# Kernel tuning notes

Measured on AMD Instinct MI355X. Metric: run time of the kernel, lower is better.

The kernel has to match this reference:

```python
import jax, jax.numpy as jnp
import numpy as np

D_MODEL = 512
D_INNER = 1024           # expand=2 * d_model
HEADDIM = 1024           # headdim = 2*hidden_dim -> nheads = 1
NHEADS = 1
D_STATE = 128            # Mamba2 default
D_CONV = 4               # Mamba2 default
CONV_DIM = D_INNER + 2 * D_STATE   # 1280
D_IN_PROJ = 2 * D_INNER + 2 * D_STATE + NHEADS  # 2305
BATCH, SEQ = 8, 2048
EPS = 1e-5


def setup_inputs() -> dict:
    key = jax.random.key(0)
    ks = jax.random.split(key, 8)
    x = jax.random.normal(ks[0], (BATCH, SEQ, D_MODEL), dtype=jnp.float32)
    rnn_state = jnp.zeros((1, BATCH, D_MODEL), dtype=jnp.float32)
    W_in = jax.random.normal(ks[1], (D_MODEL, D_IN_PROJ), dtype=jnp.float32) * 0.02
    conv_w = jax.random.normal(ks[2], (CONV_DIM, D_CONV), dtype=jnp.float32) * 0.2
    conv_b = jnp.zeros((CONV_DIM,), dtype=jnp.float32)
    dt_bias = jax.random.normal(ks[3], (NHEADS,), dtype=jnp.float32) * 0.1
    # A in (-16, -1): A_log = log(uniform(1,16))
    A_log = jnp.log(jax.random.uniform(ks[4], (NHEADS,), minval=1.0, maxval=16.0, dtype=jnp.float32))
    D = jnp.ones((NHEADS,), dtype=jnp.float32)
    norm_w = jnp.ones((D_INNER,), dtype=jnp.float32)
    W_out = jax.random.normal(ks[5], (D_INNER, D_MODEL), dtype=jnp.float32) * 0.02
    return {"x": x, "rnn_state": rnn_state, "W_in": W_in, "conv_w": conv_w,
            "conv_b": conv_b, "dt_bias": dt_bias, "A_log": A_log, "D": D,
            "norm_w": norm_w, "W_out": W_out}


def _mamba2_forward(x, W_in, conv_w, conv_b, dt_bias, A_log, D, norm_w, W_out):
    Bsz, T, _ = x.shape
    zxbcdt = x @ W_in                              # [B,T,2305]
    z = zxbcdt[..., :D_INNER]                      # [B,T,1024]
    xBC = zxbcdt[..., D_INNER:D_INNER + CONV_DIM]  # [B,T,1280]
    dt = zxbcdt[..., -NHEADS:]                     # [B,T,1]

    # causal depthwise conv1d over time, then silu
    xBC_t = jnp.transpose(xBC, (0, 2, 1))          # [B,C,T]
    w = conv_w[:, None, :]                          # [C,1,K]
    conv = jax.lax.conv_general_dilated(
        xBC_t, w, window_strides=(1,), padding=[(D_CONV - 1, 0)],
        feature_group_count=CONV_DIM, dimension_numbers=("NCH", "OIH", "NCH"))
    xBC = jax.nn.silu(jnp.transpose(conv, (0, 2, 1)) + conv_b)  # [B,T,1280]

    x_ssm = xBC[..., :D_INNER].reshape(Bsz, T, NHEADS, HEADDIM)  # [B,T,H,P]
    Bm = xBC[..., D_INNER:D_INNER + D_STATE]       # [B,T,N] (ngroups=1)
    Cm = xBC[..., -D_STATE:]                       # [B,T,N]

    dt = jax.nn.softplus(dt + dt_bias)             # [B,T,H]
    A = -jnp.exp(A_log)                            # [H]

    # selective SSM recurrence over time (time-major scan)
    xs = (jnp.transpose(x_ssm, (1, 0, 2, 3)),      # [T,B,H,P]
          jnp.transpose(dt, (1, 0, 2)),            # [T,B,H]
          jnp.transpose(Bm, (1, 0, 2)),            # [T,B,N]
          jnp.transpose(Cm, (1, 0, 2)))            # [T,B,N]
    h0 = jnp.zeros((Bsz, NHEADS, HEADDIM, D_STATE), dtype=x.dtype)

    def step(h, inp):
        xt, dtt, Bt, Ct = inp
        dA = jnp.exp(dtt * A)                      # [B,H]
        h = h * dA[:, :, None, None] + (dtt[:, :, None] * xt)[..., None] * Bt[:, None, None, :]
        y = jnp.einsum("bhpn,bn->bhp", h, Ct)
        return h, y

    _, ys = jax.lax.scan(step, h0, xs)             # ys: [T,B,H,P]
    y = jnp.transpose(ys, (1, 0, 2, 3)) + x_ssm * D[None, None, :, None]
    y = y.reshape(Bsz, T, D_INNER)

    # gated RMSNorm (norm_before_gate=False): rmsnorm(y * silu(z)) * weight
    y = y * jax.nn.silu(z)
    y = y * jax.lax.rsqrt(jnp.mean(y * y, axis=-1, keepdims=True) + EPS) * norm_w
    return y @ W_out                               # [B,T,D_MODEL]


def reference(x, rnn_state, W_in, conv_w, conv_b, dt_bias, A_log, D, norm_w, W_out):
    out = _mamba2_forward(x, W_in, conv_w, conv_b, dt_bias, A_log, D, norm_w, W_out)
    return (out, rnn_state)
```

## Files before the change

kernel.cpp:

```cpp
#include <hip/hip_runtime.h>
#include <hip/hip_bf16.h>
#include <math.h>

#define D_MODEL 512
#define D_INNER 1024
#define D_STATE 128
#define CONV_DIM (D_INNER + 2*D_STATE)
#define D_IN_PROJ (2*D_INNER + 2*D_STATE + 1)
#define NPROJ 2304
#define BATCH 8
#define SEQ 2048
#define NROWS (BATCH*SEQ)
#define CHUNK 128
#define NCHUNK (NROWS/CHUNK)
#define CPB (SEQ/CHUNK)
#define EPS_RMS 1e-5f

typedef __hip_bfloat16 bf16;
typedef __attribute__((ext_vector_type(8))) short short8;
typedef __attribute__((ext_vector_type(4))) float f32x4;

__device__ __forceinline__ float fbf(bf16 v) { return __bfloat162float(v); }
__device__ __forceinline__ bf16 tbf(float v) { return __float2bfloat16(v); }
__device__ __forceinline__ float fexp(float x) { return __expf(x); }
__device__ __forceinline__ float frcp(float x) { return __builtin_amdgcn_rcpf(x); }
__device__ __forceinline__ float fsilu(float a) { return a * frcp(1.f + fexp(-a)); }

__device__ __forceinline__ void gl2lds16(const bf16* g, bf16* l) {
    __builtin_amdgcn_global_load_lds(
        (const __attribute__((address_space(1))) unsigned int*)g,
        (__attribute__((address_space(3))) unsigned int*)l, 16, 0, 0);
}

__global__ __launch_bounds__(256) void k_prologue(
    const float* __restrict__ W_in, const float* __restrict__ W_out,
    const float* __restrict__ norm_w, const float* __restrict__ rnn,
    bf16* __restrict__ W_inbT, bf16* __restrict__ W_outbT, float* __restrict__ outTail)
{
    int b = blockIdx.x;
    if (b == 1152 + 512) {
        int tid = threadIdx.x;
        #pragma unroll
        for (int i = 0; i < 4; ++i)
            *(float4*)(outTail + (tid + i * 256) * 4) =
                *(const float4*)(rnn + (tid + i * 256) * 4);
        return;
    }
    __shared__ float tile[32][33];
    const float* src; bf16* dst; const float* scale;
    int c0, r0, sstride, C;
    if (b < 1152) {
        src = W_in; dst = W_inbT; scale = nullptr;
        c0 = (b % 16) * 32; r0 = (b / 16) * 32; sstride = D_IN_PROJ; C = D_MODEL;
    } else {
        int bb = b - 1152;
        src = W_out; dst = W_outbT; scale = norm_w;
        c0 = (bb % 32) * 32; r0 = (bb / 32) * 32; sstride = D_MODEL; C = D_INNER;
    }
    int tx = threadIdx.x & 31, ty = threadIdx.x >> 5;
    #pragma unroll
    for (int i = 0; i < 32; i += 8) {
        float s = scale ? scale[c0 + ty + i] : 1.f;
        tile[ty + i][tx] = src[(size_t)(c0 + ty + i) * sstride + (r0 + tx)] * s;
    }
    __syncthreads();
    #pragma unroll
    for (int i = 0; i < 32; i += 8)
        dst[(size_t)(r0 + ty + i) * C + (c0 + tx)] = tbf(tile[tx][ty + i]);
}

__global__ __launch_bounds__(256) void k_dtcvt(
    const float* __restrict__ x, const float* __restrict__ W_in,
    const float* __restrict__ dt_bias,
    bf16* __restrict__ xb, float* __restrict__ dts, float* __restrict__ ssq)
{
    __shared__ float wcol[D_MODEL];
    int tid = threadIdx.x;
    wcol[tid]       = W_in[(size_t)tid * D_IN_PROJ + 2304];
    wcol[tid + 256] = W_in[(size_t)(tid + 256) * D_IN_PROJ + 2304];
    __syncthreads();
    int row  = blockIdx.x * 4 + (tid >> 6);
    int lane = tid & 63;
    const float* xr = x + (size_t)row * D_MODEL;
    float4 a = *(const float4*)(xr + lane * 8);
    float4 b = *(const float4*)(xr + lane * 8 + 4);
    union { bf16 o[8]; uint4 u; } pk;
    pk.o[0]=tbf(a.x); pk.o[1]=tbf(a.y); pk.o[2]=tbf(a.z); pk.o[3]=tbf(a.w);
    pk.o[4]=tbf(b.x); pk.o[5]=tbf(b.y); pk.o[6]=tbf(b.z); pk.o[7]=tbf(b.w);
    *(uint4*)(xb + (size_t)row * D_MODEL + lane * 8) = pk.u;
    const float* wc = wcol + lane * 8;
    float s = a.x*wc[0]+a.y*wc[1]+a.z*wc[2]+a.w*wc[3]
            + b.x*wc[4]+b.y*wc[5]+b.z*wc[6]+b.w*wc[7];
    #pragma unroll
    for (int off = 32; off; off >>= 1) s += __shfl_xor(s, off);
    if (lane == 0) {
        float raw = s + dt_bias[0];
        dts[row] = raw > 20.f ? raw : log1pf(fexp(raw));
        ssq[row] = 0.f;
    }
}

template<int MODE>
__global__ __launch_bounds__(256) void k_bgemm(
    const bf16* __restrict__ A, int lda, size_t sA,
    const bf16* __restrict__ Bt, int ldb, size_t sB,
    void* __restrict__ Cv, int ldc, size_t sC, int K,
    const bf16* __restrict__ zg, float* __restrict__ ssq)
{
    constexpr int BK = 64;
    __shared__ __align__(16) bf16 SM[4 * 8192];
    const int tid = threadIdx.x, lane = tid & 63, wave = tid >> 6;
    const int wm = (wave & 1) * 64, wn = (wave >> 1) * 64;
    const int lr = lane & 15, quad = lane >> 4;
    const int rx = lr & 7;
    size_t bm, bn;
    if (MODE == 3) { bm = (size_t)blockIdx.y * 128; bn = (size_t)blockIdx.x * 128; }
    else           { bm = (size_t)blockIdx.x * 128; bn = (size_t)blockIdx.y * 128; }
    const size_t bi = blockIdx.z;
    A  += bi * sA;
    Bt += bi * sB;
    const int srow = lane >> 3;
    const int scol = (((lane & 7) ^ srow) << 3);

    f32x4 acc[4][4];
    #pragma unroll
    for (int i = 0; i < 4; ++i)
        #pragma unroll
        for (int j = 0; j < 4; ++j) acc[i][j] = (f32x4){0.f,0.f,0.f,0.f};

    auto stage = [&](bf16* Ad, bf16* Bd, int k0) {
        #pragma unroll
        for (int q = 0; q < 4; ++q) {
            int rg = wave * 32 + q * 8;
            gl2lds16(A  + (bm + rg + srow) * lda + k0 + scol, Ad + rg * BK);
            gl2lds16(Bt + (bn + rg + srow) * ldb + k0 + scol, Bd + rg * BK);
        }
    };

    const int NT = K / BK;
    stage(SM, SM + 8192, 0);
    if (NT > 1) stage(SM + 16384, SM + 24576, BK);

    for (int kt = 0; kt < NT; ++kt) {
        if (kt + 1 < NT) asm volatile("s_waitcnt vmcnt(8)" ::: "memory");
        else             asm volatile("s_waitcnt vmcnt(0)" ::: "memory");
        __builtin_amdgcn_s_barrier();
        __builtin_amdgcn_sched_barrier(0);
        const bf16* As = SM + (kt & 1) * 16384;
        const bf16* Bs = As + 8192;
        #pragma unroll
        for (int ks = 0; ks < BK; ks += 32) {
            const int off = ((((ks >> 3) + quad) ^ rx) << 3);
            short8 af[4], bg[4];
            #pragma unroll
            for (int i = 0; i < 4; ++i)
                af[i] = *(const short8*)(As + (wm + i*16 + lr) * BK + off);
            #pragma unroll
            for (int j = 0; j < 4; ++j)
                bg[j] = *(const short8*)(Bs + (wn + j*16 + lr) * BK + off);
            #pragma unroll
            for (int i = 0; i < 4; ++i)
                #pragma unroll
                for (int j = 0; j < 4; ++j)
                    acc[i][j] = __builtin_amdgcn_mfma_f32_16x16x32_bf16(af[i], bg[j], acc[i][j], 0,0,0);
        }
        __builtin_amdgcn_sched_barrier(0);
        __builtin_amdgcn_s_barrier();
        if (kt + 2 < NT) {
            bf16* An = SM + (kt & 1) * 16384;
            stage(An, An + 8192, (kt + 2) * BK);
        }
    }
    if (MODE <= 1) {
        #pragma unroll
        for (int i = 0; i < 4; ++i)
            #pragma unroll
            for (int j = 0; j < 4; ++j)
                #pragma unroll
                for (int r = 0; r < 4; ++r) {
                    size_t row = bm + wm + i*16 + quad*4 + r;
                    size_t col = bn + wn + j*16 + lr;
                    float v = acc[i][j][r];
                    if (MODE == 0) ((float*)Cv + bi*sC)[row * ldc + col] = v;
                    else           ((bf16*)Cv + bi*sC)[row * ldc + col] = tbf(v);
                }
    } else if (MODE == 2) {
        const size_t tokbase = bi * CHUNK;
        const bf16* zrow = zg + tokbase * D_INNER + bn;
        __syncthreads();
        #pragma unroll
        for (int q = 0; q < 8; ++q) {
            int r0 = wave * 32 + q * 4;
            int rr = r0 + (lane >> 4);
            int gl = (lane & 15) ^ (rr & 7);
            gl2lds16(zrow + (size_t)rr * D_INNER + gl * 8, SM + r0 * 128);
        }
        __syncthreads();
        float srw[4][4];
        #pragma unroll
        for (int i = 0; i < 4; ++i)
            #pragma unroll
            for (int r = 0; r < 4; ++r) srw[i][r] = 0.f;
        #pragma unroll
        for (int i = 0; i < 4; ++i)
            #pragma unroll
            for (int j = 0; j < 4; ++j)
                #pragma unroll
                for (int r = 0; r < 4; ++r) {
                    int row = wm + i*16 + quad*4 + r;
                    int col = wn + j*16 + lr;
                    int gph = ((col >> 3) ^ (row & 7));
                    float z = fbf(SM[row * 128 + (gph << 3) + (col & 7)]);
                    float g = acc[i][j][r] * z * frcp(1.f + fexp(-z));
                    ((bf16*)Cv + bi*sC)[(size_t)row * ldc + bn + col] = tbf(g);
                    srw[i][r] += g * g;
                }
        #pragma unroll
        for (int i = 0; i < 4; ++i)
            #pragma unroll
            for (int r = 0; r < 4; ++r) {
                float s = srw[i][r];
                s += __shfl_xor(s, 1);
                s += __shfl_xor(s, 2);
                s += __shfl_xor(s, 4);
                s += __shfl_xor(s, 8);
                if (lr == 0)
                    atomicAdd(ssq + tokbase + wm + i*16 + quad*4 + r, s);
            }
    } else {
        #pragma unroll
        for (int i = 0; i < 4; ++i)
            #pragma unroll
            for (int r = 0; r < 4; ++r) {
                size_t row = bm + wm + i*16 + quad*4 + r;
                float sc = rsqrtf(ssq[row] * (1.f / D_INNER) + EPS_RMS);
                #pragma unroll
                for (int j = 0; j < 4; ++j) {
                    size_t col = bn + wn + j*16 + lr;
                    ((float*)Cv + bi*sC)[row * ldc + col] = acc[i][j][r] * sc;
                }
            }
    }
}

__global__ __launch_bounds__(256) void k_gemm_in(
    const bf16* __restrict__ A, const bf16* __restrict__ Bt,
    bf16* __restrict__ zb, bf16* __restrict__ xBCin)
{
    constexpr int BK = 64;
    constexpr int K = D_MODEL;
    constexpr int NT = K / BK;
    __shared__ __align__(16) bf16 SM[4 * 8192];
    const int tid = threadIdx.x, lane = tid & 63, wave = tid >> 6;
    const int wm = (wave & 1) * 64, wn = (wave >> 1) * 64;
    const int lr = lane & 15, quad = lane >> 4;
    const int rx = lr & 7;
    const int bid = blockIdx.x;
    const int xcd = bid & 7, lid = bid >> 3;
    const int st  = lid / 72, r5 = lid % 72;
    const size_t bm = (size_t)(xcd * 16 + st * 4 + r5 / 18) * 128;
    const int    bn = (r5 % 18) * 128;
    const int srow = lane >> 3;
    const int scol = (((lane & 7) ^ srow) << 3);

    f32x4 acc[4][4];
    #pragma unroll
    for (int i = 0; i < 4; ++i)
        #pragma unroll
        for (int j = 0; j < 4; ++j) acc[i][j] = (f32x4){0.f,0.f,0.f,0.f};

    auto stage = [&](bf16* Ad, bf16* Bd, int k0) {
        #pragma unroll
        for (int q = 0; q < 4; ++q) {
            int rg = wave * 32 + q * 8;
            gl2lds16(A  + (bm + rg + srow) * K + k0 + scol, Ad + rg * BK);
            gl2lds16(Bt + ((size_t)bn + rg + srow) * K + k0 + scol, Bd + rg * BK);
        }
    };

    stage(SM, SM + 8192, 0);
    stage(SM + 16384, SM + 24576, BK);

    for (int kt = 0; kt < NT; ++kt) {
        if (kt + 1 < NT) asm volatile("s_waitcnt vmcnt(8)" ::: "memory");
        else             asm volatile("s_waitcnt vmcnt(0)" ::: "memory");
        __builtin_amdgcn_s_barrier();
        __builtin_amdgcn_sched_barrier(0);
        const bf16* As = SM + (kt & 1) * 16384;
        const bf16* Bs = As + 8192;
        #pragma unroll
        for (int ks = 0; ks < BK; ks += 32) {
            const int off = ((((ks >> 3) + quad) ^ rx) << 3);
            short8 af[4], bg[4];
            #pragma unroll
            for (int i = 0; i < 4; ++i)
                af[i] = *(const short8*)(As + (wm + i*16 + lr) * BK + off);
            #pragma unroll
            for (int j = 0; j < 4; ++j)
                bg[j] = *(const short8*)(Bs + (wn + j*16 + lr) * BK + off);
            #pragma unroll
            for (int i = 0; i < 4; ++i)
                #pragma unroll
                for (int j = 0; j < 4; ++j)
                    acc[i][j] = __builtin_amdgcn_mfma_f32_16x16x32_bf16(af[i], bg[j], acc[i][j], 0,0,0);
        }
        __builtin_amdgcn_sched_barrier(0);
        __builtin_amdgcn_s_barrier();
        if (kt + 2 < NT) {
            bf16* An = SM + (kt & 1) * 16384;
            stage(An, An + 8192, (kt + 2) * BK);
        }
    }
    #pragma unroll
    for (int i = 0; i < 4; ++i)
        #pragma unroll
        for (int j = 0; j < 4; ++j)
            #pragma unroll
            for (int r = 0; r < 4; ++r) {
                size_t row = bm + wm + i*16 + quad*4 + r;
                int col = bn + wn + j*16 + lr;
                float v = acc[i][j][r];
                if (col < D_INNER) zb[row * D_INNER + col] = tbf(v);
                else xBCin[row * CONV_DIM + (col - D_INNER)] = tbf(v);
            }
}

__global__ void k_prep(const float* __restrict__ dts, const float* __restrict__ A_log,
                       float* __restrict__ svec, float* __restrict__ wvec,
                       float* __restrict__ esvec, float* __restrict__ Pc)
{
    int chunk = blockIdx.x, t = threadIdx.x;
    int row = chunk * CHUNK + t;
    float A = -fexp(A_log[0]);
    __shared__ float sh[CHUNK];
    sh[t] = A * dts[row];
    __syncthreads();
    for (int off = 1; off < CHUNK; off <<= 1) {
        float v = (t >= off) ? sh[t - off] : 0.f;
        __syncthreads();
        sh[t] += v;
        __syncthreads();
    }
    float s = sh[t], sL = sh[CHUNK - 1];
    svec[row]  = s;
    wvec[row]  = fexp(sL - s) * dts[row];
    esvec[row] = fexp(s);
    if (t == CHUNK - 1) Pc[chunk] = fexp(sL);
}

__global__ __launch_bounds__(256) void k_ssd_bc(
    const bf16* __restrict__ xBCin, const float* __restrict__ conv_w,
    const float* __restrict__ conv_b, const float* __restrict__ wvec,
    const float* __restrict__ esvec, const float* __restrict__ svec,
    const float* __restrict__ dts, const float* __restrict__ Dp,
    bf16* __restrict__ Bw, bf16* __restrict__ A2)
{
    __shared__ __align__(16) bf16 Ls[131][128];
    __shared__ __align__(16) bf16 Bts[128][136];
    __shared__ __align__(16) bf16 Cts[128][136];
    __shared__ float sv_s[128], dt_s[128], wv_s[128], es_s[128];
    const int chunk = blockIdx.x;
    const int tid = threadIdx.x;
    const bool first = (chunk % CPB) == 0;
    const size_t rowbase = (size_t)chunk * CHUNK;
    if (tid < 128) {
        sv_s[tid] = svec[rowbase + tid];
        dt_s[tid] = dts[rowbase + tid];
        wv_s[tid] = wvec[rowbase + tid];
        es_s[tid] = esvec[rowbase + tid];
    }
    const int ch  = tid & 127;
    const int seg = tid >> 7;

    #pragma unroll
    for (int phase = 0; phase < 2; ++phase) {
        const int coff = D_INNER + phase * 128;
        __syncthreads();
        for (int i = tid; i < 131 * 16; i += 256) {
            int r = i >> 4, cg = (i & 15) << 3;
            uint4 v = (uint4){0,0,0,0};
            if (!(first && r < 3))
                v = *(const uint4*)(xBCin + (rowbase + r - 3) * CONV_DIM + coff + cg);
            *(uint4*)(&Ls[r][cg]) = v;
        }
        __syncthreads();
        float4 w = *(const float4*)(conv_w + (coff + ch) * 4);
        float bias = conv_b[coff + ch];
        float xv[11];
        #pragma unroll
        for (int i = 0; i < 3; ++i) xv[i + 8] = fbf(Ls[seg * 64 + i][ch]);
        for (int v = 0; v < 8; ++v) {
            int t0 = seg * 64 + v * 8;
            xv[0]=xv[8]; xv[1]=xv[9]; xv[2]=xv[10];
            #pragma unroll
            for (int i = 3; i < 11; ++i) xv[i] = fbf(Ls[t0 + i][ch]);
            float o[8];
            #pragma unroll
            for (int j = 0; j < 8; ++j) {
                float a = bias + w.x*xv[j] + w.y*xv[j+1] + w.z*xv[j+2] + w.w*xv[j+3];
                o[j] = fsilu(a);
            }
            if (phase == 0) {
                union { bf16 ob[8]; uint4 u; } pk;
                #pragma unroll
                for (int j = 0; j < 8; ++j) {
                    Bts[t0 + j][ch] = tbf(o[j]);
                    pk.ob[j] = tbf(o[j] * wv_s[t0 + j]);
                }
                *(uint4*)(Bw + (size_t)chunk*(D_STATE*CHUNK) + (size_t)ch*CHUNK + t0) = pk.u;
            } else {
                #pragma unroll
                for (int j = 0; j < 8; ++j) {
                    Cts[t0 + j][ch] = tbf(o[j]);
                    A2[(size_t)chunk*(CHUNK*256) + (size_t)(t0+j)*256 + 128 + ch] =
                        tbf(o[j] * es_s[t0 + j]);
                }
            }
        }
    }
    __syncthreads();
    const int lane = tid & 63, wave = tid >> 6;
    const int wm = (wave & 1) * 64, wn = (wave >> 1) * 64;
    const int lr = lane & 15, quad = lane >> 4;
    f32x4 acc[4][4];
    #pragma unroll
    for (int i = 0; i < 4; ++i)
        #pragma unroll
        for (int j = 0; j < 4; ++j) acc[i][j] = (f32x4){0.f,0.f,0.f,0.f};
    #pragma unroll
    for (int ks = 0; ks < 128; ks += 32) {
        short8 af[4], bg[4];
        #pragma unroll
        for (int i = 0; i < 4; ++i)
            af[i] = *(const short8*)(&Cts[wm + i*16 + lr][ks + quad*8]);
        #pragma unroll
        for (int j = 0; j < 4; ++j)
            bg[j] = *(const short8*)(&Bts[wn + j*16 + lr][ks + quad*8]);
        #pragma unroll
        for (int i = 0; i < 4; ++i)
            #pragma unroll
            for (int j = 0; j < 4; ++j)
                acc[i][j] = __builtin_amdgcn_mfma_f32_16x16x32_bf16(af[i], bg[j], acc[i][j], 0,0,0);
    }
    const float D0 = Dp[0];
    #pragma unroll
    for (int i = 0; i < 4; ++i)
        #pragma unroll
        for (int j = 0; j < 4; ++j)
            #pragma unroll
            for (int r = 0; r < 4; ++r) {
                int t = wm + i*16 + quad*4 + r;
                int u = wn + j*16 + lr;
                float o = 0.f;
                if (u <= t) {
                    o = acc[i][j][r] * fexp(sv_s[t] - sv_s[u]) * dt_s[u];
                    if (u == t) o += D0;
                }
                A2[(size_t)chunk*(CHUNK*256) + (size_t)t*256 + u] = tbf(o);
            }
}

__global__ __launch_bounds__(256) void k_conv_xdh(
    const bf16* __restrict__ xBCin, const float* __restrict__ conv_w,
    const float* __restrict__ conv_b, const bf16* __restrict__ Bw,
    bf16* __restrict__ B2, bf16* __restrict__ dH)
{
    __shared__ __align__(16) bf16 Ls[131][128];
    __shared__ __align__(16) bf16 XsF[128 * 128];
    const int chunk = blockIdx.y;
    const int p0 = blockIdx.x * 128;
    const int tid = threadIdx.x;
    const bool first = (chunk % CPB) == 0;
    const size_t rowbase = (size_t)chunk * CHUNK;
    for (int i = tid; i < 131 * 16; i += 256) {
        int r = i >> 4, cg = (i & 15) << 3;
        uint4 v = (uint4){0,0,0,0};
        if (!(first && r < 3))
            v = *(const uint4*)(xBCin + (rowbase + r - 3) * CONV_DIM + p0 + cg);
        *(uint4*)(&Ls[r][cg]) = v;
    }
    __syncthreads();
    const int p = tid & 127;
    const int half = tid >> 7;
    const int ch = p0 + p;
    float4 w = *(const float4*)(conv_w + ch * 4);
    float bias = conv_b[ch];
    bf16* outrow = B2 + (size_t)chunk * (D_INNER * 256) + (size_t)ch * 256;
    float xv[11];
    #pragma unroll
    for (int i = 0; i < 3; ++i) xv[i + 8] = fbf(Ls[half * 64 + i][p]);
    for (int v = 0; v < 8; ++v) {
        int t0 = half * 64 + v * 8;
        xv[0]=xv[8]; xv[1]=xv[9]; xv[2]=xv[10];
        #pragma unroll
        for (int i = 3; i < 11; ++i) xv[i] = fbf(Ls[t0 + i][p]);
        union { bf16 o[8]; uint4 u; } pk;
        #pragma unroll
        for (int j = 0; j < 8; ++j) {
            float a = bias + w.x*xv[j] + w.y*xv[j+1] + w.z*xv[j+2] + w.w*xv[j+3];
            pk.o[j] = tbf(fsilu(a));
        }
        *(uint4*)(outrow + t0) = pk.u;
        *(uint4*)(&XsF[p * 128 + ((((t0 >> 3) ^ (p & 7))) << 3)]) = pk.u;
    }
    __syncthreads();
    const int lane = tid & 63, wave = tid >> 6;
    const int wm = (wave & 1) * 64, wn = (wave >> 1) * 64;
    const int lr = lane & 15, quad = lane >> 4;
    const bf16* bwc = Bw + (size_t)chunk * (D_STATE * CHUNK);
    f32x4 acc[4][4];
    #pragma unroll
    for (int i = 0; i < 4; ++i)
        #pragma unroll
        for (int j = 0; j < 4; ++j) acc[i][j] = (f32x4){0.f,0.f,0.f,0.f};
    #pragma unroll
    for (int ks = 0; ks < 128; ks += 32) {
        short8 af[4], bg[4];
        #pragma unroll
        for (int j = 0; j < 4; ++j)
            bg[j] = *(const short8*)(bwc + (size_t)(wn + j*16 + lr) * CHUNK + ks + quad*8);
        #pragma unroll
        for (int i = 0; i < 4; ++i)
            af[i] = *(const short8*)(&XsF[(wm + i*16 + lr) * 128 +
                                          (((((ks >> 3) + quad) ^ (lr & 7))) << 3)]);
        #pragma unroll
        for (int i = 0; i < 4; ++i)
            #pragma unroll
            for (int j = 0; j < 4; ++j)
                acc[i][j] = __builtin_amdgcn_mfma_f32_16x16x32_bf16(af[i], bg[j], acc[i][j], 0,0,0);
    }
    #pragma unroll
    for (int i = 0; i < 4; ++i)
        #pragma unroll
        for (int j = 0; j < 4; ++j)
            #pragma unroll
            for (int r = 0; r < 4; ++r) {
                int pr = p0 + wm + i*16 + quad*4 + r;
                int n  = wn + j*16 + lr;
                dH[(size_t)chunk*(D_INNER*D_STATE) + (size_t)pr*D_STATE + n] = tbf(acc[i][j][r]);
            }
}

__global__ __launch_bounds__(256) void k_carry(
    const bf16* __restrict__ dH, const float* __restrict__ Pc, bf16* __restrict__ B2)
{
    int idx = blockIdx.x * 256 + threadIdx.x;
    int b = blockIdx.y;
    int p = idx >> 4, ng = (idx & 15) << 3;
    uint4 v[CPB];
    float pc[CPB];
    #pragma unroll
    for (int c = 0; c < CPB; ++c)
        v[c] = *(const uint4*)(dH + (size_t)(b*CPB + c)*(D_INNER*D_STATE) + (size_t)p*D_STATE + ng);
    #pragma unroll
    for (int c = 0; c < CPB; ++c) pc[c] = Pc[b*CPB + c];
    float h[8] = {0,0,0,0,0,0,0,0};
    #pragma unroll
    for (int c = 0; c < CPB; ++c) {
        union { bf16 o[8]; uint4 u; } pk;
        #pragma unroll
        for (int k = 0; k < 8; ++k) pk.o[k] = tbf(h[k]);
        *(uint4*)(B2 + (size_t)(b*CPB + c)*(D_INNER*256) + (size_t)p*256 + 128 + ng) = pk.u;
        const bf16* vb = (const bf16*)&v[c];
        #pragma unroll
        for (int k = 0; k < 8; ++k) h[k] = pc[c]*h[k] + fbf(vb[k]);
    }
}

extern "C" void kernel_launch(void* const* d_in, const int* in_sizes, int n_in,
                              void* d_out, int out_size, void* d_ws, size_t ws_size,
                              hipStream_t stream)
{
    const float* x       = (const float*)d_in[0];
    const float* rnn     = (const float*)d_in[1];
    const float* W_in    = (const float*)d_in[2];
    const float* conv_w  = (const float*)d_in[3];
    const float* conv_b  = (const float*)d_in[4];
    const float* dt_bias = (const float*)d_in[5];
    const float* A_log   = (const float*)d_in[6];
    const float* Dp      = (const float*)d_in[7];
    const float* norm_w  = (const float*)d_in[8];
    const float* W_out   = (const float*)d_in[9];
    float* out = (float*)d_out;

    char* ws = (char*)d_ws;
    size_t off = 0;
    auto alloc = [&](size_t bytes) { void* p = ws + off; off += (bytes + 255) & ~255ULL; return p; };

    bf16*  W_inbT  = (bf16*) alloc((size_t)NPROJ * D_MODEL * 2);
    bf16*  W_outbT = (bf16*) alloc((size_t)D_MODEL * D_INNER * 2);
    float* dts     = (float*)alloc((size_t)NROWS * 4);
    float* svec    = (float*)alloc((size_t)NROWS * 4);
    float* wvec    = (float*)alloc((size_t)NROWS * 4);
    float* esvec   = (float*)alloc((size_t)NROWS * 4);
    float* Pc      = (float*)alloc((size_t)NCHUNK * 4);
    float* ssq     = (float*)alloc((size_t)NROWS * 4);
    bf16*  zb      = (bf16*) alloc((size_t)NROWS * D_INNER * 2);
    bf16*  A2      = (bf16*) alloc((size_t)NCHUNK * CHUNK * 256 * 2);
    bf16*  B2      = (bf16*) alloc((size_t)NCHUNK * D_INNER * 256 * 2);
    bf16*  Bw      = (bf16*) alloc((size_t)NCHUNK * D_STATE * CHUNK * 2);
    char* RA = (char*)alloc((size_t)NROWS * D_MODEL * 2 + (size_t)NROWS * D_INNER * 2);
    bf16*  xb   = (bf16*)RA;
    bf16*  dH   = (bf16*)(RA + (size_t)NROWS * D_MODEL * 2);
    bf16*  ybf  = (bf16*)RA;
    bf16*  xBCin = (bf16*)alloc((size_t)NROWS * CONV_DIM * 2);

    k_dtcvt<<<NROWS / 4, 256, 0, stream>>>(x, W_in, dt_bias, xb, dts, ssq);
    k_prologue<<<1152 + 512 + 1, 256, 0, stream>>>(
        W_in, W_out, norm_w, rnn, W_inbT, W_outbT, out + (size_t)NROWS * D_MODEL);
    k_prep<<<NCHUNK, CHUNK, 0, stream>>>(dts, A_log, svec, wvec, esvec, Pc);

    k_gemm_in<<<dim3((NROWS/128) * (NPROJ/128)), 256, 0, stream>>>(xb, W_inbT, zb, xBCin);

    k_ssd_bc<<<NCHUNK, 256, 0, stream>>>(xBCin, conv_w, conv_b, wvec, esvec,
                                         svec, dts, Dp, Bw, A2);

    k_conv_xdh<<<dim3(8, NCHUNK), 256, 0, stream>>>(xBCin, conv_w, conv_b, Bw, B2, dH);

    k_carry<<<dim3(64, BATCH), 256, 0, stream>>>(dH, Pc, B2);

    k_bgemm<2><<<dim3(1, D_INNER/128, NCHUNK), 256, 0, stream>>>(
        A2, 256, (size_t)CHUNK*256,
        B2, 256, (size_t)D_INNER*256,
        ybf, D_INNER, (size_t)CHUNK*D_INNER, 256, zb, ssq);

    k_bgemm<3><<<dim3(D_MODEL/128, NROWS/128, 1), 256, 0, stream>>>(
        ybf, D_INNER, 0, W_outbT, D_INNER, 0, out, D_MODEL, 0, D_INNER,
        nullptr, ssq);
}
```

Measured before the change: 293.2 us.

## Use 512-thread GEMM blocks with 4-stage LDS prefetch pipeline

The GEMM kernels (input projection, chunked SSD bgemm, output projection) move from 4 waves each computing 64x64 to 8 waves each computing 32x64 of a 128x128 tile. The LDS ring grows from 2 to 4 stages (128 KB), so three K-tiles stay in flight, with matching vmcnt waits. The output GEMM grid is reordered so the row tile comes from blockIdx.x. The goal is more latency hiding and more waves per CU. The cost is higher LDS use that may limit co-resident blocks, and less data reuse per wave.

Measured after the change: 307.7 us. +5.0%, slower.

```diff
diff --git a/kernel.cpp b/kernel.cpp
--- a/kernel.cpp
+++ b/kernel.cpp
@@ -101,79 +101,79 @@
 }
 
 template<int MODE>
-__global__ __launch_bounds__(256) void k_bgemm(
+__global__ __launch_bounds__(512, 2) void k_bgemm(
     const bf16* __restrict__ A, int lda, size_t sA,
     const bf16* __restrict__ Bt, int ldb, size_t sB,
     void* __restrict__ Cv, int ldc, size_t sC, int K,
     const bf16* __restrict__ zg, float* __restrict__ ssq)
 {
     constexpr int BK = 64;
-    __shared__ __align__(16) bf16 SM[4 * 8192];
+    __shared__ __align__(16) bf16 SM[4 * 16384];
     const int tid = threadIdx.x, lane = tid & 63, wave = tid >> 6;
-    const int wm = (wave & 1) * 64, wn = (wave >> 1) * 64;
+    const int wm = (wave & 3) * 32, wn = (wave >> 2) * 64;
     const int lr = lane & 15, quad = lane >> 4;
     const int rx = lr & 7;
-    size_t bm, bn;
-    if (MODE == 3) { bm = (size_t)blockIdx.y * 128; bn = (size_t)blockIdx.x * 128; }
-    else           { bm = (size_t)blockIdx.x * 128; bn = (size_t)blockIdx.y * 128; }
+    const size_t bm = (size_t)blockIdx.x * 128;
+    const size_t bn = (size_t)blockIdx.y * 128;
     const size_t bi = blockIdx.z;
     A  += bi * sA;
     Bt += bi * sB;
     const int srow = lane >> 3;
     const int scol = (((lane & 7) ^ srow) << 3);
 
-    f32x4 acc[4][4];
-    #pragma unroll
-    for (int i = 0; i < 4; ++i)
+    f32x4 acc[2][4];
+    #pragma unroll
+    for (int i = 0; i < 2; ++i)
         #pragma unroll
         for (int j = 0; j < 4; ++j) acc[i][j] = (f32x4){0.f,0.f,0.f,0.f};
 
-    auto stage = [&](bf16* Ad, bf16* Bd, int k0) {
-        #pragma unroll
-        for (int q = 0; q < 4; ++q) {
-            int rg = wave * 32 + q * 8;
+    auto stage = [&](int buf, int k0) {
+        bf16* Ad = SM + buf * 16384;
+        bf16* Bd = Ad + 8192;
+        #pragma unroll
+        for (int q = 0; q < 2; ++q) {
+            int rg = q * 64 + wave * 8;
             gl2lds16(A  + (bm + rg + srow) * lda + k0 + scol, Ad + rg * BK);
             gl2lds16(Bt + (bn + rg + srow) * ldb + k0 + scol, Bd + rg * BK);
         }
     };
 
     const int NT = K / BK;
-    stage(SM, SM + 8192, 0);
-    if (NT > 1) stage(SM + 16384, SM + 24576, BK);
+    stage(0, 0); stage(1, BK); stage(2, 2 * BK); stage(3, 3 * BK);
 
     for (int kt = 0; kt < NT; ++kt) {
-        if (kt + 1 < NT) asm volatile("s_waitcnt vmcnt(8)" ::: "memory");
-        else             asm volatile("s_waitcnt vmcnt(0)" ::: "memory");
+        const int rem = NT - 1 - kt;
+        if (rem >= 3)      asm volatile("s_waitcnt vmcnt(12)" ::: "memory");
+        else if (rem == 2) asm volatile("s_waitcnt vmcnt(8)"  ::: "memory");
+        else if (rem == 1) asm volatile("s_waitcnt vmcnt(4)"  ::: "memory");
+        else               asm volatile("s_waitcnt vmcnt(0)"  ::: "memory");
         __builtin_amdgcn_s_barrier();
         __builtin_amdgcn_sched_barrier(0);
-        const bf16* As = SM + (kt & 1) * 16384;
+        const bf16* As = SM + (kt & 3) * 16384;
         const bf16* Bs = As + 8192;
         #pragma unroll
         for (int ks = 0; ks < BK; ks += 32) {
             const int off = ((((ks >> 3) + quad) ^ rx) << 3);
-            short8 af[4], bg[4];
-            #pragma unroll
-            for (int i = 0; i < 4; ++i)
+            short8 af[2], bg[4];
+            #pragma unroll
+            for (int i = 0; i < 2; ++i)
                 af[i] = *(const short8*)(As + (wm + i*16 + lr) * BK + off);
             #pragma unroll
             for (int j = 0; j < 4; ++j)
                 bg[j] = *(const short8*)(Bs + (wn + j*16 + lr) * BK + off);
             #pragma unroll
-            for (int i = 0; i < 4; ++i)
+            for (int i = 0; i < 2; ++i)
                 #pragma unroll
                 for (int j = 0; j < 4; ++j)
                     acc[i][j] = __builtin_amdgcn_mfma_f32_16x16x32_bf16(af[i], bg[j], acc[i][j], 0,0,0);
         }
         __builtin_amdgcn_sched_barrier(0);
         __builtin_amdgcn_s_barrier();
-        if (kt + 2 < NT) {
-            bf16* An = SM + (kt & 1) * 16384;
-            stage(An, An + 8192, (kt + 2) * BK);
-        }
+        if (kt + 4 < NT) stage(kt & 3, (kt + 4) * BK);
     }
     if (MODE <= 1) {
         #pragma unroll
-        for (int i = 0; i < 4; ++i)
+        for (int i = 0; i < 2; ++i)
             #pragma unroll
             for (int j = 0; j < 4; ++j)
                 #pragma unroll
@@ -189,20 +189,20 @@
         const bf16* zrow = zg + tokbase * D_INNER + bn;
         __syncthreads();
         #pragma unroll
-        for (int q = 0; q < 8; ++q) {
-            int r0 = wave * 32 + q * 4;
+        for (int q = 0; q < 4; ++q) {
+            int r0 = wave * 16 + q * 4;
             int rr = r0 + (lane >> 4);
             int gl = (lane & 15) ^ (rr & 7);
             gl2lds16(zrow + (size_t)rr * D_INNER + gl * 8, SM + r0 * 128);
         }
         __syncthreads();
-        float srw[4][4];
-        #pragma unroll
-        for (int i = 0; i < 4; ++i)
+        float srw[2][4];
+        #pragma unroll
+        for (int i = 0; i < 2; ++i)
             #pragma unroll
             for (int r = 0; r < 4; ++r) srw[i][r] = 0.f;
         #pragma unroll
-        for (int i = 0; i < 4; ++i)
+        for (int i = 0; i < 2; ++i)
             #pragma unroll
             for (int j = 0; j < 4; ++j)
                 #pragma unroll
@@ -216,7 +216,7 @@
                     srw[i][r] += g * g;
                 }
         #pragma unroll
-        for (int i = 0; i < 4; ++i)
+        for (int i = 0; i < 2; ++i)
             #pragma unroll
             for (int r = 0; r < 4; ++r) {
                 float s = srw[i][r];
@@ -229,7 +229,7 @@
             }
     } else {
         #pragma unroll
-        for (int i = 0; i < 4; ++i)
+        for (int i = 0; i < 2; ++i)
             #pragma unroll
             for (int r = 0; r < 4; ++r) {
                 size_t row = bm + wm + i*16 + quad*4 + r;
@@ -243,16 +243,16 @@
     }
 }
 
-__global__ __launch_bounds__(256) void k_gemm_in(
+__global__ __launch_bounds__(512, 2) void k_gemm_in(
     const bf16* __restrict__ A, const bf16* __restrict__ Bt,
     bf16* __restrict__ zb, bf16* __restrict__ xBCin)
 {
     constexpr int BK = 64;
     constexpr int K = D_MODEL;
     constexpr int NT = K / BK;
-    __shared__ __align__(16) bf16 SM[4 * 8192];
+    __shared__ __align__(16) bf16 SM[4 * 16384];
     const int tid = threadIdx.x, lane = tid & 63, wave = tid >> 6;
-    const int wm = (wave & 1) * 64, wn = (wave >> 1) * 64;
+    const int wm = (wave & 3) * 32, wn = (wave >> 2) * 64;
     const int lr = lane & 15, quad = lane >> 4;
     const int rx = lr & 7;
     const int bid = blockIdx.x;
@@ -263,56 +263,57 @@
     const int srow = lane >> 3;
     const int scol = (((lane & 7) ^ srow) << 3);
 
-    f32x4 acc[4][4];
-    #pragma unroll
-    for (int i = 0; i < 4; ++i)
+    f32x4 acc[2][4];
+    #pragma unroll
+    for (int i = 0; i < 2; ++i)
         #pragma unroll
         for (int j = 0; j < 4; ++j) acc[i][j] = (f32x4){0.f,0.f,0.f,0.f};
 
-    auto stage = [&](bf16* Ad, bf16* Bd, int k0) {
-        #pragma unroll
-        for (int q = 0; q < 4; ++q) {
-            int rg = wave * 32 + q * 8;
+    auto stage = [&](int buf, int k0) {
+        bf16* Ad = SM + buf * 16384;
+        bf16* Bd = Ad + 8192;
+        #pragma unroll
+        for (int q = 0; q < 2; ++q) {
+            int rg = q * 64 + wave * 8;
             gl2lds16(A  + (bm + rg + srow) * K + k0 + scol, Ad + rg * BK);
             gl2lds16(Bt + ((size_t)bn + rg + srow) * K + k0 + scol, Bd + rg * BK);
         }
     };
 
-    stage(SM, SM + 8192, 0);
-    stage(SM + 16384, SM + 24576, BK);
+    stage(0, 0); stage(1, BK); stage(2, 2 * BK); stage(3, 3 * BK);
 
     for (int kt = 0; kt < NT; ++kt) {
-        if (kt + 1 < NT) asm volatile("s_waitcnt vmcnt(8)" ::: "memory");
-        else             asm volatile("s_waitcnt vmcnt(0)" ::: "memory");
+        const int rem = NT - 1 - kt;
+        if (rem >= 3)      asm volatile("s_waitcnt vmcnt(12)" ::: "memory");
+        else if (rem == 2) asm volatile("s_waitcnt vmcnt(8)"  ::: "memory");
+        else if (rem == 1) asm volatile("s_waitcnt vmcnt(4)"  ::: "memory");
+        else               asm volatile("s_waitcnt vmcnt(0)"  ::: "memory");
         __builtin_amdgcn_s_barrier();
         __builtin_amdgcn_sched_barrier(0);
-        const bf16* As = SM + (kt & 1) * 16384;
+        const bf16* As = SM + (kt & 3) * 16384;
         const bf16* Bs = As + 8192;
         #pragma unroll
         for (int ks = 0; ks < BK; ks += 32) {
             const int off = ((((ks >> 3) + quad) ^ rx) << 3);
-            short8 af[4], bg[4];
-            #pragma unroll
-            for (int i = 0; i < 4; ++i)
+            short8 af[2], bg[4];
+            #pragma unroll
+            for (int i = 0; i < 2; ++i)
                 af[i] = *(const short8*)(As + (wm + i*16 + lr) * BK + off);
             #pragma unroll
             for (int j = 0; j < 4; ++j)
                 bg[j] = *(const short8*)(Bs + (wn + j*16 + lr) * BK + off);
             #pragma unroll
-            for (int i = 0; i < 4; ++i)
+            for (int i = 0; i < 2; ++i)
                 #pragma unroll
                 for (int j = 0; j < 4; ++j)
                     acc[i][j] = __builtin_amdgcn_mfma_f32_16x16x32_bf16(af[i], bg[j], acc[i][j], 0,0,0);
         }
         __builtin_amdgcn_sched_barrier(0);
         __builtin_amdgcn_s_barrier();
-        if (kt + 2 < NT) {
-            bf16* An = SM + (kt & 1) * 16384;
-            stage(An, An + 8192, (kt + 2) * BK);
-        }
-    }
-    #pragma unroll
-    for (int i = 0; i < 4; ++i)
+        if (kt + 4 < NT) stage(kt & 3, (kt + 4) * BK);
+    }
+    #pragma unroll
+    for (int i = 0; i < 2; ++i)
         #pragma unroll
         for (int j = 0; j < 4; ++j)
             #pragma unroll
@@ -610,7 +611,7 @@
         W_in, W_out, norm_w, rnn, W_inbT, W_outbT, out + (size_t)NROWS * D_MODEL);
     k_prep<<<NCHUNK, CHUNK, 0, stream>>>(dts, A_log, svec, wvec, esvec, Pc);
 
-    k_gemm_in<<<dim3((NROWS/128) * (NPROJ/128)), 256, 0, stream>>>(xb, W_inbT, zb, xBCin);
+    k_gemm_in<<<dim3((NROWS/128) * (NPROJ/128)), 512, 0, stream>>>(xb, W_inbT, zb, xBCin);
 
     k_ssd_bc<<<NCHUNK, 256, 0, stream>>>(xBCin, conv_w, conv_b, wvec, esvec,
                                          svec, dts, Dp, Bw, A2);
@@ -619,12 +620,12 @@
 
     k_carry<<<dim3(64, BATCH), 256, 0, stream>>>(dH, Pc, B2);
 
-    k_bgemm<2><<<dim3(1, D_INNER/128, NCHUNK), 256, 0, stream>>>(
+    k_bgemm<2><<<dim3(1, D_INNER/128, NCHUNK), 512, 0, stream>>>(
         A2, 256, (size_t)CHUNK*256,
         B2, 256, (size_t)D_INNER*256,
         ybf, D_INNER, (size_t)CHUNK*D_INNER, 256, zb, ssq);
 
-    k_bgemm<3><<<dim3(D_MODEL/128, NROWS/128, 1), 256, 0, stream>>>(
+    k_bgemm<3><<<dim3(NROWS/128, D_MODEL/128, 1), 512, 0, stream>>>(
         ybf, D_INNER, 0, W_outbT, D_INNER, 0, out, D_MODEL, 0, D_INNER,
         nullptr, ssq);
 }
```

## Deepen input-projection GEMM pipeline to 4 stages with BK=32 and swap out-proj grid order

Applied to the files above, without the earlier changes.

The input projection GEMM moves from a 2-stage double buffer with BK=64 to a 4-stage ring with BK=32. The LDS footprint stays the same, and a new XOR swizzle and graded vmcnt waits let up to three tiles be in flight while MFMAs run. The output-projection GEMM's grid is transposed so blockIdx.x walks M tiles, which changes which blocks share W_out and A tiles in cache. The trade-off is more barriers per unit of K work and a different L2 reuse pattern in the out-projection.

After: 299.7 us. +2.2%, slower.

```diff
diff --git a/kernel.cpp b/kernel.cpp
--- a/kernel.cpp
+++ b/kernel.cpp
@@ -113,9 +113,8 @@
     const int wm = (wave & 1) * 64, wn = (wave >> 1) * 64;
     const int lr = lane & 15, quad = lane >> 4;
     const int rx = lr & 7;
-    size_t bm, bn;
-    if (MODE == 3) { bm = (size_t)blockIdx.y * 128; bn = (size_t)blockIdx.x * 128; }
-    else           { bm = (size_t)blockIdx.x * 128; bn = (size_t)blockIdx.y * 128; }
+    const size_t bm = (size_t)blockIdx.x * 128;
+    const size_t bn = (size_t)blockIdx.y * 128;
     const size_t bi = blockIdx.z;
     A  += bi * sA;
     Bt += bi * sB;
@@ -247,21 +246,21 @@
     const bf16* __restrict__ A, const bf16* __restrict__ Bt,
     bf16* __restrict__ zb, bf16* __restrict__ xBCin)
 {
-    constexpr int BK = 64;
+    constexpr int BK = 32;
     constexpr int K = D_MODEL;
     constexpr int NT = K / BK;
-    __shared__ __align__(16) bf16 SM[4 * 8192];
+    __shared__ __align__(16) bf16 SM[8 * 4096];
     const int tid = threadIdx.x, lane = tid & 63, wave = tid >> 6;
     const int wm = (wave & 1) * 64, wn = (wave >> 1) * 64;
     const int lr = lane & 15, quad = lane >> 4;
-    const int rx = lr & 7;
     const int bid = blockIdx.x;
     const int xcd = bid & 7, lid = bid >> 3;
     const int st  = lid / 72, r5 = lid % 72;
     const size_t bm = (size_t)(xcd * 16 + st * 4 + r5 / 18) * 128;
     const int    bn = (r5 % 18) * 128;
-    const int srow = lane >> 3;
-    const int scol = (((lane & 7) ^ srow) << 3);
+    const int srow = lane >> 2;
+    const int scol = (((lane & 3) ^ ((srow >> 1) & 3)) << 3);
+    const int gread = ((quad ^ ((lr >> 1) & 3)) << 3);
 
     f32x4 acc[4][4];
     #pragma unroll
@@ -269,47 +268,44 @@
         #pragma unroll
         for (int j = 0; j < 4; ++j) acc[i][j] = (f32x4){0.f,0.f,0.f,0.f};
 
-    auto stage = [&](bf16* Ad, bf16* Bd, int k0) {
-        #pragma unroll
-        for (int q = 0; q < 4; ++q) {
-            int rg = wave * 32 + q * 8;
+    auto stage = [&](int buf, int k0) {
+        bf16* Ad = SM + buf * 8192;
+        bf16* Bd = Ad + 4096;
+        #pragma unroll
+        for (int q = 0; q < 2; ++q) {
+            int rg = wave * 32 + q * 16;
             gl2lds16(A  + (bm + rg + srow) * K + k0 + scol, Ad + rg * BK);
             gl2lds16(Bt + ((size_t)bn + rg + srow) * K + k0 + scol, Bd + rg * BK);
         }
     };
 
-    stage(SM, SM + 8192, 0);
-    stage(SM + 16384, SM + 24576, BK);
+    stage(0, 0); stage(1, BK); stage(2, 2 * BK); stage(3, 3 * BK);
 
     for (int kt = 0; kt < NT; ++kt) {
-        if (kt + 1 < NT) asm volatile("s_waitcnt vmcnt(8)" ::: "memory");
-        else             asm volatile("s_waitcnt vmcnt(0)" ::: "memory");
+        const int rem = NT - 1 - kt;
+        if (rem >= 3)      asm volatile("s_waitcnt vmcnt(12)" ::: "memory");
+        else if (rem == 2) asm volatile("s_waitcnt vmcnt(8)"  ::: "memory");
+        else if (rem == 1) asm volatile("s_waitcnt vmcnt(4)"  ::: "memory");
+        else               asm volatile("s_waitcnt vmcnt(0)"  ::: "memory");
         __builtin_amdgcn_s_barrier();
         __builtin_amdgcn_sched_barrier(0);
-        const bf16* As = SM + (kt & 1) * 16384;
-        const bf16* Bs = As + 8192;
-        #pragma unroll
-        for (int ks = 0; ks < BK; ks += 32) {
-            const int off = ((((ks >> 3) + quad) ^ rx) << 3);
-            short8 af[4], bg[4];
-            #pragma unroll
-            for (int i = 0; i < 4; ++i)
-                af[i] = *(const short8*)(As + (wm + i*16 + lr) * BK + off);
+        const bf16* As = SM + (kt & 3) * 8192;
+        const bf16* Bs = As + 4096;
+        short8 af[4], bg[4];
+        #pragma unroll
+        for (int i = 0; i < 4; ++i)
+            af[i] = *(const short8*)(As + (wm + i*16 + lr) * BK + gread);
+        #pragma unroll
+        for (int j = 0; j < 4; ++j)
+            bg[j] = *(const short8*)(Bs + (wn + j*16 + lr) * BK + gread);
+        #pragma unroll
+        for (int i = 0; i < 4; ++i)
             #pragma unroll
             for (int j = 0; j < 4; ++j)
-                bg[j] = *(const short8*)(Bs + (wn + j*16 + lr) * BK + off);
-            #pragma unroll
-            for (int i = 0; i < 4; ++i)
-                #pragma unroll
-                for (int j = 0; j < 4; ++j)
-                    acc[i][j] = __builtin_amdgcn_mfma_f32_16x16x32_bf16(af[i], bg[j], acc[i][j], 0,0,0);
-        }
+                acc[i][j] = __builtin_amdgcn_mfma_f32_16x16x32_bf16(af[i], bg[j], acc[i][j], 0,0,0);
         __builtin_amdgcn_sched_barrier(0);
         __builtin_amdgcn_s_barrier();
-        if (kt + 2 < NT) {
-            bf16* An = SM + (kt & 1) * 16384;
-            stage(An, An + 8192, (kt + 2) * BK);
-        }
+        if (kt + 4 < NT) stage(kt & 3, (kt + 4) * BK);
     }
     #pragma unroll
     for (int i = 0; i < 4; ++i)
@@ -624,7 +620,7 @@
         B2, 256, (size_t)D_INNER*256,
         ybf, D_INNER, (size_t)CHUNK*D_INNER, 256, zb, ssq);
 
-    k_bgemm<3><<<dim3(D_MODEL/128, NROWS/128, 1), 256, 0, stream>>>(
+    k_bgemm<3><<<dim3(NROWS/128, D_MODEL/128, 1), 256, 0, stream>>>(
         ybf, D_INNER, 0, W_outbT, D_INNER, 0, out, D_MODEL, 0, D_INNER,
         nullptr, ssq);
 }
```
